# Kernel tuning notes

Hardware: AMD Instinct MI355X
Metric: run time of the kernel (lower is better)

Reference implementation:

```python
import jax, jax.numpy as jnp
import numpy as np

B, S, EH2, DH, A = 128, 1024, 1024, 512, 512

def setup_inputs() -> dict:
    key = jax.random.key(0)
    k1, k2, k3, k4, k5 = jax.random.split(key, 5)
    scale_in = 1.0 / np.sqrt(EH2 + DH)
    scale_a = 1.0 / np.sqrt(A)
    return {
        "encoder_outputs": jax.random.normal(k1, (B, S, EH2), dtype=jnp.float32),
        "decoder_hidden": jax.random.normal(k2, (B, DH), dtype=jnp.float32),
        "src_mask": jnp.ones((B, S), dtype=jnp.int32),
        "W_attn": jax.random.normal(k3, (EH2 + DH, A), dtype=jnp.float32) * scale_in,
        "b_attn": jax.random.normal(k4, (A,), dtype=jnp.float32) * scale_in,
        "v": jax.random.normal(k5, (A,), dtype=jnp.float32) * scale_a,
    }

def reference(encoder_outputs, decoder_hidden, src_mask, W_attn, b_attn, v):
    # Split W_attn into encoder-part and decoder-part to avoid materializing
    # the [B,S,EH2+DH] concat (same math as Linear(cat(enc, dec_repeated))).
    W_enc = W_attn[:EH2]          # [EH2, A]
    W_dec = W_attn[EH2:]          # [DH, A]
    enc_proj = jnp.einsum('bse,ea->bsa', encoder_outputs, W_enc)  # [B,S,A]
    dec_proj = decoder_hidden @ W_dec                              # [B,A]
    energy = jnp.tanh(enc_proj + dec_proj[:, None, :] + b_attn)    # [B,S,A]
    scores = jnp.einsum('bsa,a->bs', energy, v)                    # [B,S]
    scores = jnp.where(src_mask == 0, jnp.float32(-1e10), scores)
    attn_weights = jax.nn.softmax(scores, axis=1)                  # [B,S]
    context = jnp.einsum('bs,bse->be', attn_weights, encoder_outputs)  # [B,EH2]
    return (context, attn_weights)
```

## Files before the change

### kernel.cpp

```cpp
#include <hip/hip_runtime.h>
#include <math.h>

#define BB   128
#define SS   1024
#define EH2  1024
#define DHD  512
#define AD   512
#define MTOT (BB*SS)
#define KDIM 1024

#define BM2   128
#define BK2   32
#define NSTEP (KDIM/BK2)

typedef __attribute__((ext_vector_type(8)))  short short8;
typedef __attribute__((ext_vector_type(4)))  float f32x4;
typedef __attribute__((ext_vector_type(16))) float f32x16;

static __device__ __forceinline__ unsigned short f2bf_rne(float x) {
    unsigned u = __float_as_uint(x);
    u += 0x7FFF + ((u >> 16) & 1);
    return (unsigned short)(u >> 16);
}

#define LDS_AS(p) ((__attribute__((address_space(3))) unsigned int*)(p))
#define GLB_AS(p) ((const __attribute__((address_space(1))) unsigned int*)(p))

__global__ __launch_bounds__(256) void k0_wprep(
    const float* __restrict__ W, unsigned short* __restrict__ Wt)
{
    const int g     = blockIdx.x * 256 + threadIdx.x;
    const int lane  = g & 63;
    const int ct    = (g >> 6) & 15;
    const int kk2   = (g >> 10) & 1;
    const int ks    = g >> 11;
    const int col   = ct * 32 + (lane & 31);
    const int kbase = ks * 32 + kk2 * 16 + (lane >> 5) * 8;
    short8 out;
    #pragma unroll
    for (int j = 0; j < 8; ++j)
        out[j] = (short)f2bf_rne(W[(size_t)(kbase + j) * AD + col]);
    *(short8*)&Wt[(size_t)g * 8] = out;
}

__global__ __launch_bounds__(256) void k1_decproj(
    const float* __restrict__ dec,
    const float* __restrict__ Wdec,
    const float* __restrict__ bias,
    float* __restrict__ dec_proj)
{
    __shared__ float dls[DHD];
    const int b = blockIdx.x;
    const int t = threadIdx.x;
    for (int i = t; i < DHD; i += 256) dls[i] = dec[b * DHD + i];
    __syncthreads();
    float acc0 = bias[t];
    float acc1 = bias[t + 256];
    #pragma unroll 8
    for (int k = 0; k < DHD; ++k) {
        const float d = dls[k];
        acc0 += d * Wdec[(size_t)k * AD + t];
        acc1 += d * Wdec[(size_t)k * AD + t + 256];
    }
    dec_proj[b * AD + t]       = acc0;
    dec_proj[b * AD + t + 256] = acc1;
}

__global__ __launch_bounds__(512, 2) void k2_gemm_score(
    const float* __restrict__ enc,
    const unsigned short* __restrict__ Wt,
    const float* __restrict__ dp,
    const float* __restrict__ v,
    float* __restrict__ scores)
{
    __shared__ unsigned short As[2][16][512];
    __shared__ unsigned short Bs[2][32][512];
    __shared__ float dp_l[AD], v_l[AD];
    __shared__ float sred[4][BM2];

    const int t     = threadIdx.x;
    const int wave  = t >> 6;
    const int lane  = t & 63;
    const int mbase = blockIdx.x * BM2;
    const int b     = blockIdx.x >> 3;
    const int wm    = wave >> 2;
    const int wn    = wave & 3;

    dp_l[t] = dp[b * AD + t];
    v_l[t]  = v[t];

    const int smt   = (t >> 6) & 3;
    const int skk2  = t >> 8;
    const int srow  = smt * 32 + (lane & 31);
    const int sksub = skk2 * 16 + (lane >> 5) * 8;
    const float* aptr = enc + (size_t)(mbase + srow) * KDIM + sksub;
    unsigned short* asH = &As[0][skk2 * 4 + smt][lane * 8];
    unsigned short* asL = &As[0][(2 + skk2) * 4 + smt][lane * 8];
    const int asStride = 16 * 512;

    const unsigned short* bsrc = Wt + (size_t)wave * 2048 + (size_t)lane * 8;
    unsigned short* bdst = &Bs[0][wave * 4][0];
    const int bsStride = 32 * 512;

#define STAGE_B(ks_, buf_) do {                                             \
    const unsigned short* gs_ = bsrc + (size_t)(ks_) * 16384;               \
    unsigned short* ds_ = bdst + (buf_) * bsStride;                         \
    __builtin_amdgcn_global_load_lds(GLB_AS(gs_),        LDS_AS(ds_),        16, 0, 0); \
    __builtin_amdgcn_global_load_lds(GLB_AS(gs_ + 512),  LDS_AS(ds_ + 512),  16, 0, 0); \
    __builtin_amdgcn_global_load_lds(GLB_AS(gs_ + 1024), LDS_AS(ds_ + 1024), 16, 0, 0); \
    __builtin_amdgcn_global_load_lds(GLB_AS(gs_ + 1536), LDS_AS(ds_ + 1536), 16, 0, 0); \
} while (0)

#define CONV_WRITE_A(buf_, xa_, xb_) do {                                   \
    const float xs_[8] = {xa_.x, xa_.y, xa_.z, xa_.w, xb_.x, xb_.y, xb_.z, xb_.w}; \
    short8 hi_, lo_;                                                        \
    _Pragma("unroll")                                                       \
    for (int j_ = 0; j_ < 8; ++j_) {                                        \
        const unsigned u_ = __float_as_uint(xs_[j_]);                       \
        hi_[j_] = (short)(u_ >> 16);                                        \
        lo_[j_] = (short)f2bf_rne(xs_[j_] - __uint_as_float(u_ & 0xFFFF0000u)); \
    }                                                                       \
    *(short8*)(asH + (buf_) * asStride) = hi_;                              \
    *(short8*)(asL + (buf_) * asStride) = lo_;                              \
} while (0)

    f32x16 acc[2][4];
    #pragma unroll
    for (int mi = 0; mi < 2; ++mi)
        #pragma unroll
        for (int n = 0; n < 4; ++n) acc[mi][n] = (f32x16)0.f;

    STAGE_B(0, 0);
    {
        const float4 xa = *(const float4*)(aptr);
        const float4 xb = *(const float4*)(aptr + 4);
        CONV_WRITE_A(0, xa, xb);
    }
    __syncthreads();

    int cur = 0;
    for (int ks = 0; ks < NSTEP; ++ks) {
        const int nxt = cur ^ 1;
        float4 xa, xb;
        const bool pf = (ks + 1 < NSTEP);
        if (pf) {
            STAGE_B(ks + 1, nxt);
            xa = *(const float4*)(aptr + (ks + 1) * BK2);
            xb = *(const float4*)(aptr + (ks + 1) * BK2 + 4);
        }

        #pragma unroll
        for (int kk2 = 0; kk2 < 2; ++kk2) {
            short8 bf[4];
            #pragma unroll
            for (int n = 0; n < 4; ++n)
                bf[n] = *(const short8*)&Bs[cur][kk2 * 16 + wn * 4 + n][lane * 8];
            #pragma unroll
            for (int mi = 0; mi < 2; ++mi) {
                const int mt = wm * 2 + mi;
                const short8 aH = *(const short8*)&As[cur][kk2 * 4 + mt][lane * 8];
                const short8 aL = *(const short8*)&As[cur][(2 + kk2) * 4 + mt][lane * 8];
                #pragma unroll
                for (int n = 0; n < 4; ++n) {
                    acc[mi][n] = __builtin_amdgcn_mfma_f32_32x32x16_bf16(aH, bf[n], acc[mi][n], 0, 0, 0);
                    acc[mi][n] = __builtin_amdgcn_mfma_f32_32x32x16_bf16(aL, bf[n], acc[mi][n], 0, 0, 0);
                }
            }
        }

        if (pf) CONV_WRITE_A(nxt, xa, xb);
        __syncthreads();
        cur = nxt;
    }

    const int c    = lane & 31;
    const int half = lane >> 5;
    float vv[4], dpv[4];
    #pragma unroll
    for (int n = 0; n < 4; ++n) {
        const int col = wn * 128 + n * 32 + c;
        vv[n]  = v_l[col];
        dpv[n] = dp_l[col];
    }
    #pragma unroll
    for (int mi = 0; mi < 2; ++mi) {
        const int mt = wm * 2 + mi;
        float part[16];
        #pragma unroll
        for (int r = 0; r < 16; ++r) {
            float s = 0.f;
            #pragma unroll
            for (int n = 0; n < 4; ++n) {
                const float e  = acc[mi][n][r] + dpv[n];
                const float te = __expf(2.f * e);
                s += vv[n] * (1.f - __fdividef(2.f, te + 1.f));
            }
            part[r] = s;
        }
        #pragma unroll
        for (int off = 1; off < 32; off <<= 1)
            #pragma unroll
            for (int r = 0; r < 16; ++r)
                part[r] += __shfl_xor(part[r], off);
        if (c == 0) {
            #pragma unroll
            for (int r = 0; r < 16; ++r)
                sred[wn][mt * 32 + 4 * half + (r & 3) + 8 * (r >> 2)] = part[r];
        }
    }
    __syncthreads();
    if (t < BM2)
        scores[mbase + t] = sred[0][t] + sred[1][t] + sred[2][t] + sred[3][t];
#undef STAGE_B
#undef CONV_WRITE_A
}

__global__ __launch_bounds__(256) void k3_softmax(
    const float* __restrict__ sc,
    const int*   __restrict__ mask,
    float* __restrict__ wts)
{
    const int b = blockIdx.x;
    const int t = threadIdx.x;
    float local[4];
    float mx = -3.0e38f;
    #pragma unroll
    for (int r = 0; r < 4; ++r) {
        const int s = r * 256 + t;
        float val = sc[b * SS + s];
        if (mask[b * SS + s] == 0) val = -1.0e10f;
        local[r] = val;
        mx = fmaxf(mx, val);
    }
    #pragma unroll
    for (int off = 1; off < 64; off <<= 1) mx = fmaxf(mx, __shfl_xor(mx, off));
    __shared__ float redm[4], reds[4];
    if ((t & 63) == 0) redm[t >> 6] = mx;
    __syncthreads();
    mx = fmaxf(fmaxf(redm[0], redm[1]), fmaxf(redm[2], redm[3]));

    float sum = 0.f;
    #pragma unroll
    for (int r = 0; r < 4; ++r) { local[r] = __expf(local[r] - mx); sum += local[r]; }
    #pragma unroll
    for (int off = 1; off < 64; off <<= 1) sum += __shfl_xor(sum, off);
    if ((t & 63) == 0) reds[t >> 6] = sum;
    __syncthreads();
    sum = reds[0] + reds[1] + reds[2] + reds[3];
    const float inv = 1.f / sum;
    #pragma unroll
    for (int r = 0; r < 4; ++r) wts[b * SS + r * 256 + t] = local[r] * inv;
}

#define SCHUNK 128
__global__ __launch_bounds__(256) void k4_context(
    const float* __restrict__ enc,
    const float* __restrict__ wts,
    float* __restrict__ ctx)
{
    const int b  = blockIdx.x;
    const int ch = blockIdx.y;
    const int e4 = threadIdx.x * 4;
    const float* encb = enc + (size_t)b * SS * EH2 + (size_t)ch * SCHUNK * EH2;
    const float* wb   = wts + b * SS + ch * SCHUNK;
    float4 acc = make_float4(0.f, 0.f, 0.f, 0.f);
    #pragma unroll 4
    for (int s = 0; s < SCHUNK; ++s) {
        const float w = wb[s];
        const float4 ev = *(const float4*)&encb[(size_t)s * EH2 + e4];
        acc.x = fmaf(w, ev.x, acc.x);
        acc.y = fmaf(w, ev.y, acc.y);
        acc.z = fmaf(w, ev.z, acc.z);
        acc.w = fmaf(w, ev.w, acc.w);
    }
    atomicAdd(&ctx[b * EH2 + e4 + 0], acc.x);
    atomicAdd(&ctx[b * EH2 + e4 + 1], acc.y);
    atomicAdd(&ctx[b * EH2 + e4 + 2], acc.z);
    atomicAdd(&ctx[b * EH2 + e4 + 3], acc.w);
}

extern "C" void kernel_launch(void* const* d_in, const int* in_sizes, int n_in,
                              void* d_out, int out_size, void* d_ws, size_t ws_size,
                              hipStream_t stream) {
    const float* enc    = (const float*)d_in[0];
    const float* dec    = (const float*)d_in[1];
    const int*   mask   = (const int*)  d_in[2];
    const float* W      = (const float*)d_in[3];
    const float* b_attn = (const float*)d_in[4];
    const float* v      = (const float*)d_in[5];

    float* out = (float*)d_out;
    float* ctx = out;
    float* wts = out + BB * EH2;

    unsigned short* Wt  = (unsigned short*)d_ws;
    float* dec_proj     = (float*)((char*)d_ws + (1 << 20));
    float* scores       = dec_proj + BB * AD;

    hipMemsetAsync(ctx, 0, (size_t)BB * EH2 * sizeof(float), stream);

    k0_wprep<<<256, 256, 0, stream>>>(W, Wt);

    k1_decproj<<<BB, 256, 0, stream>>>(dec, W + (size_t)EH2 * AD, b_attn, dec_proj);

    k2_gemm_score<<<MTOT / BM2, 512, 0, stream>>>(enc, Wt, dec_proj, v, scores);

    k3_softmax<<<BB, 256, 0, stream>>>(scores, mask, wts);

    dim3 g4(BB, SS / SCHUNK);
    k4_context<<<g4, 256, 0, stream>>>(enc, wts, ctx);
}
```

Before: 1.036 ms.

## Read W fragments straight from global memory and halve the GEMM M tile

```diff
diff --git a/kernel.cpp b/kernel.cpp
--- a/kernel.cpp
+++ b/kernel.cpp
@@ -9,12 +9,11 @@
 #define MTOT (BB*SS)
 #define KDIM 1024
 
-#define BM2   128
+#define BM2   64
 #define BK2   32
 #define NSTEP (KDIM/BK2)
 
 typedef __attribute__((ext_vector_type(8)))  short short8;
-typedef __attribute__((ext_vector_type(4)))  float f32x4;
 typedef __attribute__((ext_vector_type(16))) float f32x16;
 
 static __device__ __forceinline__ unsigned short f2bf_rne(float x) {
@@ -22,9 +21,6 @@
     u += 0x7FFF + ((u >> 16) & 1);
     return (unsigned short)(u >> 16);
 }
-
-#define LDS_AS(p) ((__attribute__((address_space(3))) unsigned int*)(p))
-#define GLB_AS(p) ((const __attribute__((address_space(1))) unsigned int*)(p))
 
 __global__ __launch_bounds__(256) void k0_wprep(
     const float* __restrict__ W, unsigned short* __restrict__ Wt)
@@ -66,50 +62,40 @@
     dec_proj[b * AD + t + 256] = acc1;
 }
 
-__global__ __launch_bounds__(512, 2) void k2_gemm_score(
+#define AS_IDX(hl, kk2, mt) (((hl) * 2 + (kk2)) * 2 + (mt))
+
+__global__ __launch_bounds__(256, 2) void k2_gemm_score(
     const float* __restrict__ enc,
     const unsigned short* __restrict__ Wt,
     const float* __restrict__ dp,
     const float* __restrict__ v,
     float* __restrict__ scores)
 {
-    __shared__ unsigned short As[2][16][512];
-    __shared__ unsigned short Bs[2][32][512];
+    __shared__ unsigned short As[2][8][512];
     __shared__ float dp_l[AD], v_l[AD];
     __shared__ float sred[4][BM2];
 
     const int t     = threadIdx.x;
-    const int wave  = t >> 6;
+    const int wn    = t >> 6;
     const int lane  = t & 63;
     const int mbase = blockIdx.x * BM2;
-    const int b     = blockIdx.x >> 3;
-    const int wm    = wave >> 2;
-    const int wn    = wave & 3;
-
-    dp_l[t] = dp[b * AD + t];
-    v_l[t]  = v[t];
-
-    const int smt   = (t >> 6) & 3;
-    const int skk2  = t >> 8;
-    const int srow  = smt * 32 + (lane & 31);
-    const int sksub = skk2 * 16 + (lane >> 5) * 8;
-    const float* aptr = enc + (size_t)(mbase + srow) * KDIM + sksub;
-    unsigned short* asH = &As[0][skk2 * 4 + smt][lane * 8];
-    unsigned short* asL = &As[0][(2 + skk2) * 4 + smt][lane * 8];
-    const int asStride = 16 * 512;
-
-    const unsigned short* bsrc = Wt + (size_t)wave * 2048 + (size_t)lane * 8;
-    unsigned short* bdst = &Bs[0][wave * 4][0];
-    const int bsStride = 32 * 512;
-
-#define STAGE_B(ks_, buf_) do {                                             \
-    const unsigned short* gs_ = bsrc + (size_t)(ks_) * 16384;               \
-    unsigned short* ds_ = bdst + (buf_) * bsStride;                         \
-    __builtin_amdgcn_global_load_lds(GLB_AS(gs_),        LDS_AS(ds_),        16, 0, 0); \
-    __builtin_amdgcn_global_load_lds(GLB_AS(gs_ + 512),  LDS_AS(ds_ + 512),  16, 0, 0); \
-    __builtin_amdgcn_global_load_lds(GLB_AS(gs_ + 1024), LDS_AS(ds_ + 1024), 16, 0, 0); \
-    __builtin_amdgcn_global_load_lds(GLB_AS(gs_ + 1536), LDS_AS(ds_ + 1536), 16, 0, 0); \
-} while (0)
+    const int b     = blockIdx.x >> 4;
+
+    dp_l[t]       = dp[b * AD + t];
+    dp_l[t + 256] = dp[b * AD + t + 256];
+    v_l[t]        = v[t];
+    v_l[t + 256]  = v[t + 256];
+
+    const int smt  = (t >> 6) & 1;
+    const int skk2 = t >> 7;
+    const int srow = smt * 32 + (lane & 31);
+    const int skb  = skk2 * 16 + (lane >> 5) * 8;
+    const float* aptr = enc + (size_t)(mbase + srow) * KDIM + skb;
+    unsigned short* asH = &As[0][AS_IDX(0, skk2, smt)][lane * 8];
+    unsigned short* asL = &As[0][AS_IDX(1, skk2, smt)][lane * 8];
+    const int asStride = 8 * 512;
+
+    const short8* bbase = (const short8*)Wt + wn * 256 + lane;
 
 #define CONV_WRITE_A(buf_, xa_, xb_) do {                                   \
     const float xs_[8] = {xa_.x, xa_.y, xa_.z, xa_.w, xb_.x, xb_.y, xb_.z, xb_.w}; \
@@ -130,7 +116,6 @@
         #pragma unroll
         for (int n = 0; n < 4; ++n) acc[mi][n] = (f32x16)0.f;
 
-    STAGE_B(0, 0);
     {
         const float4 xa = *(const float4*)(aptr);
         const float4 xb = *(const float4*)(aptr + 4);
@@ -138,40 +123,62 @@
     }
     __syncthreads();
 
-    int cur = 0;
-    for (int ks = 0; ks < NSTEP; ++ks) {
-        const int nxt = cur ^ 1;
-        float4 xa, xb;
-        const bool pf = (ks + 1 < NSTEP);
-        if (pf) {
-            STAGE_B(ks + 1, nxt);
-            xa = *(const float4*)(aptr + (ks + 1) * BK2);
-            xb = *(const float4*)(aptr + (ks + 1) * BK2 + 4);
-        }
-
-        #pragma unroll
-        for (int kk2 = 0; kk2 < 2; ++kk2) {
-            short8 bf[4];
-            #pragma unroll
-            for (int n = 0; n < 4; ++n)
-                bf[n] = *(const short8*)&Bs[cur][kk2 * 16 + wn * 4 + n][lane * 8];
-            #pragma unroll
-            for (int mi = 0; mi < 2; ++mi) {
-                const int mt = wm * 2 + mi;
-                const short8 aH = *(const short8*)&As[cur][kk2 * 4 + mt][lane * 8];
-                const short8 aL = *(const short8*)&As[cur][(2 + kk2) * 4 + mt][lane * 8];
-                #pragma unroll
-                for (int n = 0; n < 4; ++n) {
-                    acc[mi][n] = __builtin_amdgcn_mfma_f32_32x32x16_bf16(aH, bf[n], acc[mi][n], 0, 0, 0);
-                    acc[mi][n] = __builtin_amdgcn_mfma_f32_32x32x16_bf16(aL, bf[n], acc[mi][n], 0, 0, 0);
-                }
-            }
-        }
-
-        if (pf) CONV_WRITE_A(nxt, xa, xb);
-        __syncthreads();
-        cur = nxt;
-    }
+#define KSTEP(BUF, ks_)                                                      \
+  {                                                                          \
+    const bool pf = ((ks_) + 1 < NSTEP);                                     \
+    float4 xa, xb;                                                           \
+    if (pf) {                                                                \
+        xa = *(const float4*)(aptr + ((ks_) + 1) * BK2);                     \
+        xb = *(const float4*)(aptr + ((ks_) + 1) * BK2 + 4);                 \
+    }                                                                        \
+                                                                \
+    {                                                                        \
+        short8 bfr[4];                                                       \
+        _Pragma("unroll")                                                    \
+        for (int n = 0; n < 4; ++n) bfr[n] = bbase[(ks_) * 2048 + n * 64];   \
+        const short8 aH0 = *(const short8*)&As[BUF][AS_IDX(0,0,0)][lane*8];  \
+        const short8 aL0 = *(const short8*)&As[BUF][AS_IDX(1,0,0)][lane*8];  \
+        const short8 aH1 = *(const short8*)&As[BUF][AS_IDX(0,0,1)][lane*8];  \
+        const short8 aL1 = *(const short8*)&As[BUF][AS_IDX(1,0,1)][lane*8];  \
+        __builtin_amdgcn_s_setprio(1);                                       \
+        _Pragma("unroll")                                                    \
+        for (int n = 0; n < 4; ++n) {                                        \
+            acc[0][n] = __builtin_amdgcn_mfma_f32_32x32x16_bf16(aH0, bfr[n], acc[0][n], 0, 0, 0); \
+            acc[0][n] = __builtin_amdgcn_mfma_f32_32x32x16_bf16(aL0, bfr[n], acc[0][n], 0, 0, 0); \
+            acc[1][n] = __builtin_amdgcn_mfma_f32_32x32x16_bf16(aH1, bfr[n], acc[1][n], 0, 0, 0); \
+            acc[1][n] = __builtin_amdgcn_mfma_f32_32x32x16_bf16(aL1, bfr[n], acc[1][n], 0, 0, 0); \
+        }                                                                    \
+        __builtin_amdgcn_s_setprio(0);                                       \
+    }                                                                        \
+                                                                \
+    {                                                                        \
+        short8 bfr[4];                                                       \
+        _Pragma("unroll")                                                    \
+        for (int n = 0; n < 4; ++n) bfr[n] = bbase[(ks_) * 2048 + 1024 + n * 64]; \
+        const short8 aH0 = *(const short8*)&As[BUF][AS_IDX(0,1,0)][lane*8];  \
+        const short8 aL0 = *(const short8*)&As[BUF][AS_IDX(1,1,0)][lane*8];  \
+        const short8 aH1 = *(const short8*)&As[BUF][AS_IDX(0,1,1)][lane*8];  \
+        const short8 aL1 = *(const short8*)&As[BUF][AS_IDX(1,1,1)][lane*8];  \
+        __builtin_amdgcn_s_setprio(1);                                       \
+        _Pragma("unroll")                                                    \
+        for (int n = 0; n < 4; ++n) {                                        \
+            acc[0][n] = __builtin_amdgcn_mfma_f32_32x32x16_bf16(aH0, bfr[n], acc[0][n], 0, 0, 0); \
+            acc[0][n] = __builtin_amdgcn_mfma_f32_32x32x16_bf16(aL0, bfr[n], acc[0][n], 0, 0, 0); \
+            acc[1][n] = __builtin_amdgcn_mfma_f32_32x32x16_bf16(aH1, bfr[n], acc[1][n], 0, 0, 0); \
+            acc[1][n] = __builtin_amdgcn_mfma_f32_32x32x16_bf16(aL1, bfr[n], acc[1][n], 0, 0, 0); \
+        }                                                                    \
+        __builtin_amdgcn_s_setprio(0);                                       \
+    }                                                                        \
+    if (pf) CONV_WRITE_A((BUF) ^ 1, xa, xb);                                 \
+    __syncthreads();                                                         \
+  }
+
+    for (int ks = 0; ks < NSTEP; ks += 2) {
+        KSTEP(0, ks);
+        KSTEP(1, ks + 1);
+    }
+#undef KSTEP
+#undef CONV_WRITE_A
 
     const int c    = lane & 31;
     const int half = lane >> 5;
@@ -184,7 +191,6 @@
     }
     #pragma unroll
     for (int mi = 0; mi < 2; ++mi) {
-        const int mt = wm * 2 + mi;
         float part[16];
         #pragma unroll
         for (int r = 0; r < 16; ++r) {
@@ -205,14 +211,12 @@
         if (c == 0) {
             #pragma unroll
             for (int r = 0; r < 16; ++r)
-                sred[wn][mt * 32 + 4 * half + (r & 3) + 8 * (r >> 2)] = part[r];
+                sred[wn][mi * 32 + 4 * half + (r & 3) + 8 * (r >> 2)] = part[r];
         }
     }
     __syncthreads();
     if (t < BM2)
         scores[mbase + t] = sred[0][t] + sred[1][t] + sred[2][t] + sred[3][t];
-#undef STAGE_B
-#undef CONV_WRITE_A
 }
 
 __global__ __launch_bounds__(256) void k3_softmax(
@@ -303,7 +307,7 @@
 
     k1_decproj<<<BB, 256, 0, stream>>>(dec, W + (size_t)EH2 * AD, b_attn, dec_proj);
 
-    k2_gemm_score<<<MTOT / BM2, 512, 0, stream>>>(enc, Wt, dec_proj, v, scores);
+    k2_gemm_score<<<MTOT / BM2, 256, 0, stream>>>(enc, Wt, dec_proj, v, scores);
 
     k3_softmax<<<BB, 256, 0, stream>>>(scores, mask, wts);
 
```

Result: no change. 1.028 ms (-0.8%).

## Restructure score GEMM to 4 waves with B operand loaded straight into registers

Applied to the files above, without the earlier changes.

```diff
diff --git a/kernel.cpp b/kernel.cpp
--- a/kernel.cpp
+++ b/kernel.cpp
@@ -14,7 +14,6 @@
 #define NSTEP (KDIM/BK2)
 
 typedef __attribute__((ext_vector_type(8)))  short short8;
-typedef __attribute__((ext_vector_type(4)))  float f32x4;
 typedef __attribute__((ext_vector_type(16))) float f32x16;
 
 static __device__ __forceinline__ unsigned short f2bf_rne(float x) {
@@ -22,9 +21,6 @@
     u += 0x7FFF + ((u >> 16) & 1);
     return (unsigned short)(u >> 16);
 }
-
-#define LDS_AS(p) ((__attribute__((address_space(3))) unsigned int*)(p))
-#define GLB_AS(p) ((const __attribute__((address_space(1))) unsigned int*)(p))
 
 __global__ __launch_bounds__(256) void k0_wprep(
     const float* __restrict__ W, unsigned short* __restrict__ Wt)
@@ -66,7 +62,7 @@
     dec_proj[b * AD + t + 256] = acc1;
 }
 
-__global__ __launch_bounds__(512, 2) void k2_gemm_score(
+__global__ __launch_bounds__(256, 1) void k2_gemm_score(
     const float* __restrict__ enc,
     const unsigned short* __restrict__ Wt,
     const float* __restrict__ dp,
@@ -74,104 +70,115 @@
     float* __restrict__ scores)
 {
     __shared__ unsigned short As[2][16][512];
-    __shared__ unsigned short Bs[2][32][512];
     __shared__ float dp_l[AD], v_l[AD];
     __shared__ float sred[4][BM2];
 
     const int t     = threadIdx.x;
-    const int wave  = t >> 6;
+    const int wn    = t >> 6;
     const int lane  = t & 63;
     const int mbase = blockIdx.x * BM2;
     const int b     = blockIdx.x >> 3;
-    const int wm    = wave >> 2;
-    const int wn    = wave & 3;
-
-    dp_l[t] = dp[b * AD + t];
-    v_l[t]  = v[t];
-
-    const int smt   = (t >> 6) & 3;
-    const int skk2  = t >> 8;
-    const int srow  = smt * 32 + (lane & 31);
-    const int sksub = skk2 * 16 + (lane >> 5) * 8;
-    const float* aptr = enc + (size_t)(mbase + srow) * KDIM + sksub;
-    unsigned short* asH = &As[0][skk2 * 4 + smt][lane * 8];
-    unsigned short* asL = &As[0][(2 + skk2) * 4 + smt][lane * 8];
-    const int asStride = 16 * 512;
-
-    const unsigned short* bsrc = Wt + (size_t)wave * 2048 + (size_t)lane * 8;
-    unsigned short* bdst = &Bs[0][wave * 4][0];
-    const int bsStride = 32 * 512;
-
-#define STAGE_B(ks_, buf_) do {                                             \
-    const unsigned short* gs_ = bsrc + (size_t)(ks_) * 16384;               \
-    unsigned short* ds_ = bdst + (buf_) * bsStride;                         \
-    __builtin_amdgcn_global_load_lds(GLB_AS(gs_),        LDS_AS(ds_),        16, 0, 0); \
-    __builtin_amdgcn_global_load_lds(GLB_AS(gs_ + 512),  LDS_AS(ds_ + 512),  16, 0, 0); \
-    __builtin_amdgcn_global_load_lds(GLB_AS(gs_ + 1024), LDS_AS(ds_ + 1024), 16, 0, 0); \
-    __builtin_amdgcn_global_load_lds(GLB_AS(gs_ + 1536), LDS_AS(ds_ + 1536), 16, 0, 0); \
+
+    dp_l[t]       = dp[b * AD + t];
+    dp_l[t + 256] = dp[b * AD + t + 256];
+    v_l[t]        = v[t];
+    v_l[t + 256]  = v[t + 256];
+
+    const int smt  = wn;
+    const int srow = smt * 32 + (lane & 31);
+    const int so   = (lane >> 5) * 8;
+    const float* aptr = enc + (size_t)(mbase + srow) * KDIM + so;
+
+    const short8* bb8 = (const short8*)Wt + wn * 256 + lane;
+
+    float4 pA0[4], pA1[4];
+    short8 bcur[8], bnx[8];
+
+#define LOADA(ks_, SET) do {                                                \
+    const float* p_ = aptr + (ks_) * BK2;                                   \
+    SET[0] = *(const float4*)(p_);                                          \
+    SET[1] = *(const float4*)(p_ + 4);                                      \
+    SET[2] = *(const float4*)(p_ + 16);                                     \
+    SET[3] = *(const float4*)(p_ + 20);                                     \
 } while (0)
 
-#define CONV_WRITE_A(buf_, xa_, xb_) do {                                   \
-    const float xs_[8] = {xa_.x, xa_.y, xa_.z, xa_.w, xb_.x, xb_.y, xb_.z, xb_.w}; \
-    short8 hi_, lo_;                                                        \
+#define LOADB(ks_, R) do {                                                  \
     _Pragma("unroll")                                                       \
-    for (int j_ = 0; j_ < 8; ++j_) {                                        \
-        const unsigned u_ = __float_as_uint(xs_[j_]);                       \
-        hi_[j_] = (short)(u_ >> 16);                                        \
-        lo_[j_] = (short)f2bf_rne(xs_[j_] - __uint_as_float(u_ & 0xFFFF0000u)); \
+    for (int q_ = 0; q_ < 8; ++q_)                                          \
+        R[q_] = bb8[(ks_) * 2048 + (q_ >> 2) * 1024 + (q_ & 3) * 64];       \
+} while (0)
+
+#define CONVA(SET, buf_) do {                                               \
+    _Pragma("unroll")                                                       \
+    for (int kk2_ = 0; kk2_ < 2; ++kk2_) {                                  \
+        const float4 xa_ = SET[kk2_ * 2];                                   \
+        const float4 xb_ = SET[kk2_ * 2 + 1];                               \
+        const float xs_[8] = {xa_.x, xa_.y, xa_.z, xa_.w,                   \
+                              xb_.x, xb_.y, xb_.z, xb_.w};                  \
+        short8 hi_, lo_;                                                    \
+        _Pragma("unroll")                                                   \
+        for (int j_ = 0; j_ < 8; ++j_) {                                    \
+            const unsigned u_ = __float_as_uint(xs_[j_]);                   \
+            hi_[j_] = (short)(u_ >> 16);                                    \
+            lo_[j_] = (short)f2bf_rne(xs_[j_] - __uint_as_float(u_ & 0xFFFF0000u)); \
+        }                                                                   \
+        *(short8*)&As[buf_][kk2_ * 4 + smt][lane * 8]       = hi_;          \
+        *(short8*)&As[buf_][(2 + kk2_) * 4 + smt][lane * 8] = lo_;          \
     }                                                                       \
-    *(short8*)(asH + (buf_) * asStride) = hi_;                              \
-    *(short8*)(asL + (buf_) * asStride) = lo_;                              \
 } while (0)
 
-    f32x16 acc[2][4];
-    #pragma unroll
-    for (int mi = 0; mi < 2; ++mi)
+#define MFMA_STEP(BUF, BREG) do {                                           \
+    _Pragma("unroll")                                                       \
+    for (int kk2_ = 0; kk2_ < 2; ++kk2_) {                                  \
+        short8 aH_[4], aL_[4];                                              \
+        _Pragma("unroll")                                                   \
+        for (int mt_ = 0; mt_ < 4; ++mt_) {                                 \
+            aH_[mt_] = *(const short8*)&As[BUF][kk2_ * 4 + mt_][lane * 8];  \
+            aL_[mt_] = *(const short8*)&As[BUF][(2 + kk2_) * 4 + mt_][lane * 8]; \
+        }                                                                   \
+        _Pragma("unroll")                                                   \
+        for (int mt_ = 0; mt_ < 4; ++mt_)                                   \
+            _Pragma("unroll")                                               \
+            for (int n_ = 0; n_ < 4; ++n_)                                  \
+                acc[mt_][n_] = __builtin_amdgcn_mfma_f32_32x32x16_bf16(     \
+                    aH_[mt_], BREG[kk2_ * 4 + n_], acc[mt_][n_], 0, 0, 0);  \
+        _Pragma("unroll")                                                   \
+        for (int mt_ = 0; mt_ < 4; ++mt_)                                   \
+            _Pragma("unroll")                                               \
+            for (int n_ = 0; n_ < 4; ++n_)                                  \
+                acc[mt_][n_] = __builtin_amdgcn_mfma_f32_32x32x16_bf16(     \
+                    aL_[mt_], BREG[kk2_ * 4 + n_], acc[mt_][n_], 0, 0, 0);  \
+    }                                                                       \
+} while (0)
+
+    f32x16 acc[4][4];
+    #pragma unroll
+    for (int mt = 0; mt < 4; ++mt)
         #pragma unroll
-        for (int n = 0; n < 4; ++n) acc[mi][n] = (f32x16)0.f;
-
-    STAGE_B(0, 0);
-    {
-        const float4 xa = *(const float4*)(aptr);
-        const float4 xb = *(const float4*)(aptr + 4);
-        CONV_WRITE_A(0, xa, xb);
-    }
-    __syncthreads();
-
-    int cur = 0;
-    for (int ks = 0; ks < NSTEP; ++ks) {
-        const int nxt = cur ^ 1;
-        float4 xa, xb;
-        const bool pf = (ks + 1 < NSTEP);
-        if (pf) {
-            STAGE_B(ks + 1, nxt);
-            xa = *(const float4*)(aptr + (ks + 1) * BK2);
-            xb = *(const float4*)(aptr + (ks + 1) * BK2 + 4);
-        }
-
-        #pragma unroll
-        for (int kk2 = 0; kk2 < 2; ++kk2) {
-            short8 bf[4];
-            #pragma unroll
-            for (int n = 0; n < 4; ++n)
-                bf[n] = *(const short8*)&Bs[cur][kk2 * 16 + wn * 4 + n][lane * 8];
-            #pragma unroll
-            for (int mi = 0; mi < 2; ++mi) {
-                const int mt = wm * 2 + mi;
-                const short8 aH = *(const short8*)&As[cur][kk2 * 4 + mt][lane * 8];
-                const short8 aL = *(const short8*)&As[cur][(2 + kk2) * 4 + mt][lane * 8];
-                #pragma unroll
-                for (int n = 0; n < 4; ++n) {
-                    acc[mi][n] = __builtin_amdgcn_mfma_f32_32x32x16_bf16(aH, bf[n], acc[mi][n], 0, 0, 0);
-                    acc[mi][n] = __builtin_amdgcn_mfma_f32_32x32x16_bf16(aL, bf[n], acc[mi][n], 0, 0, 0);
-                }
-            }
-        }
-
-        if (pf) CONV_WRITE_A(nxt, xa, xb);
+        for (int n = 0; n < 4; ++n) acc[mt][n] = (f32x16)0.f;
+
+    LOADA(0, pA0);
+    LOADA(1, pA1);
+    LOADB(0, bcur);
+    CONVA(pA0, 0);
+    __syncthreads();
+
+    for (int ks = 0; ks < NSTEP; ks += 2) {
+        if (ks + 1 < NSTEP) LOADB(ks + 1, bnx);
+        if (ks + 2 < NSTEP) LOADA(ks + 2, pA0);
+        MFMA_STEP(0, bcur);
+        if (ks + 1 < NSTEP) CONVA(pA1, 1);
         __syncthreads();
-        cur = nxt;
-    }
+        if (ks + 2 < NSTEP) LOADB(ks + 2, bcur);
+        if (ks + 3 < NSTEP) LOADA(ks + 3, pA1);
+        MFMA_STEP(1, bnx);
+        if (ks + 2 < NSTEP) CONVA(pA0, 0);
+        __syncthreads();
+    }
+#undef LOADA
+#undef LOADB
+#undef CONVA
+#undef MFMA_STEP
 
     const int c    = lane & 31;
     const int half = lane >> 5;
@@ -183,15 +190,14 @@
         dpv[n] = dp_l[col];
     }
     #pragma unroll
-    for (int mi = 0; mi < 2; ++mi) {
-        const int mt = wm * 2 + mi;
+    for (int mt = 0; mt < 4; ++mt) {
         float part[16];
         #pragma unroll
         for (int r = 0; r < 16; ++r) {
             float s = 0.f;
             #pragma unroll
             for (int n = 0; n < 4; ++n) {
-                const float e  = acc[mi][n][r] + dpv[n];
+                const float e  = acc[mt][n][r] + dpv[n];
                 const float te = __expf(2.f * e);
                 s += vv[n] * (1.f - __fdividef(2.f, te + 1.f));
             }
@@ -211,8 +217,6 @@
     __syncthreads();
     if (t < BM2)
         scores[mbase + t] = sred[0][t] + sred[1][t] + sred[2][t] + sred[3][t];
-#undef STAGE_B
-#undef CONV_WRITE_A
 }
 
 __global__ __launch_bounds__(256) void k3_softmax(
@@ -252,7 +256,7 @@
     for (int r = 0; r < 4; ++r) wts[b * SS + r * 256 + t] = local[r] * inv;
 }
 
-#define SCHUNK 128
+#define SCHUNK 64
 __global__ __launch_bounds__(256) void k4_context(
     const float* __restrict__ enc,
     const float* __restrict__ wts,
@@ -303,7 +307,7 @@
 
     k1_decproj<<<BB, 256, 0, stream>>>(dec, W + (size_t)EH2 * AD, b_attn, dec_proj);
 
-    k2_gemm_score<<<MTOT / BM2, 512, 0, stream>>>(enc, Wt, dec_proj, v, scores);
+    k2_gemm_score<<<MTOT / BM2, 256, 0, stream>>>(enc, Wt, dec_proj, v, scores);
 
     k3_softmax<<<BB, 256, 0, stream>>>(scores, mask, wts);
 
```

Result: slower. 1.325 ms (+27.9%).
